# Kernel tuning notes

Hardware: AMD Instinct MI355X
Metric: run time of the kernel (lower is better)

## Reference

```python
import jax, jax.numpy as jnp
import numpy as np

B, T, D, H = 2, 2048, 1024, 16


def setup_inputs() -> dict:
    key = jax.random.key(0)
    kx, kq, kk, kv, ko = jax.random.split(key, 5)
    s = D ** -0.5  # linear-layer init scale
    return {
        "x": jax.random.normal(kx, (B, T, D), dtype=jnp.float32),
        "Wq": jax.random.normal(kq, (D, D), dtype=jnp.float32) * s,
        "Wk": jax.random.normal(kk, (D, D), dtype=jnp.float32) * s,
        "Wv": jax.random.normal(kv, (D, D), dtype=jnp.float32) * s,
        "Wo": jax.random.normal(ko, (D, D), dtype=jnp.float32) * s,
        "quadrant_weights": jnp.array([1.0, -0.5, -0.5, 0.25], dtype=jnp.float32),
    }


def reference(x, Wq, Wk, Wv, Wo, quadrant_weights):
    Bx, Tx, Dx = x.shape
    d = Dx // H          # head dim
    h = d // 2           # quadrant (half-head) dim
    scale = h ** -0.5

    # projections -> (B, H, T, d)
    q = (x @ Wq).reshape(Bx, Tx, H, d).transpose(0, 2, 1, 3)
    k = (x @ Wk).reshape(Bx, Tx, H, d).transpose(0, 2, 1, 3)
    v = (x @ Wv).reshape(Bx, Tx, H, d).transpose(0, 2, 1, 3)

    q1, q2 = q[..., :h], q[..., h:]
    k1, k2 = k[..., :h], k[..., h:]

    w = jax.nn.softmax(quadrant_weights)
    # Fused quadrant sum: w0*q1k1^T + w1*q1k2^T + w2*q2k1^T + w3*q2k2^T
    # == q1 @ (w0*k1 + w1*k2)^T + q2 @ (w2*k1 + w3*k2)^T  (same math, fewer matmuls)
    k_eff1 = w[0] * k1 + w[1] * k2
    k_eff2 = w[2] * k1 + w[3] * k2
    attn = (jnp.einsum('bhqc,bhkc->bhqk', q1, k_eff1)
            + jnp.einsum('bhqc,bhkc->bhqk', q2, k_eff2)) * scale
    attn = jax.nn.softmax(attn, axis=-1)

    out = jnp.einsum('bhqk,bhkd->bhqd', attn, v)
    out = out.transpose(0, 2, 1, 3).reshape(Bx, Tx, Dx)
    return out @ Wo
```

## Files before the change

kernel.cpp:

```cpp
#include <hip/hip_runtime.h>

typedef unsigned short u16;
typedef unsigned int u32;
typedef __attribute__((ext_vector_type(8))) short short8;
typedef __attribute__((ext_vector_type(4))) short short4v;
typedef __attribute__((ext_vector_type(4))) float f32x4;
typedef __attribute__((ext_vector_type(16))) float f32x16;
typedef __attribute__((ext_vector_type(2))) unsigned u32x2;
typedef __attribute__((ext_vector_type(4))) unsigned u32x4;

__device__ __forceinline__ u16 f2bf(float f) {
  union { float f; unsigned u; } a; a.f = f;
  unsigned u = a.u + 0x7fffu + ((a.u >> 16) & 1u);
  return (u16)(u >> 16);
}

__device__ __forceinline__ u32 cvtpk(float lo, float hi_) {
  u32 r; asm("v_cvt_pk_bf16_f32 %0, %1, %2" : "=v"(r) : "v"(lo), "v"(hi_)); return r;
}
__device__ __forceinline__ short8 as_short8(u32x4 v) {
  union { u32x4 u; short8 s; } c; c.u = v; return c.s;
}
__device__ __forceinline__ u32 sh32(u32 v) {
  return (u32)__shfl_xor((int)v, 32, 64);
}
__device__ __forceinline__ float max3f(float a, float b, float c) {
  return fmaxf(fmaxf(a, b), c);
}
__device__ __forceinline__ void gload16(const u16* g, u16* l) {
  __builtin_amdgcn_global_load_lds(
      (__attribute__((address_space(1))) void*)(u16*)g,
      (__attribute__((address_space(3))) void*)l, 16, 0, 0);
}
__device__ __forceinline__ void keep8(short8 v) {
  union { short8 s; int i[4]; } u; u.s = v;
  asm volatile("" :: "v"(u.i[0]), "v"(u.i[1]), "v"(u.i[2]), "v"(u.i[3]));
}
__device__ __forceinline__ void wait_vm4() {
  asm volatile("s_waitcnt vmcnt(4)" ::: "memory");
}
__device__ __forceinline__ void wait_vm3() {
  asm volatile("s_waitcnt vmcnt(3)" ::: "memory");
}
__device__ __forceinline__ void wait_vm0() {
  asm volatile("s_waitcnt vmcnt(0)" ::: "memory");
}
__device__ __forceinline__ void barrier_raw() {
  __builtin_amdgcn_sched_barrier(0);
  __builtin_amdgcn_s_barrier();
  __builtin_amdgcn_sched_barrier(0);
}

__global__ void cvt_x_kernel(const float* __restrict__ x, u16* __restrict__ xb) {
  int i = (blockIdx.x * 256 + threadIdx.x) * 8;
  float4 a = *(const float4*)(x + i);
  float4 b = *(const float4*)(x + i + 4);
  short8 v;
  v[0] = (short)f2bf(a.x); v[1] = (short)f2bf(a.y);
  v[2] = (short)f2bf(a.z); v[3] = (short)f2bf(a.w);
  v[4] = (short)f2bf(b.x); v[5] = (short)f2bf(b.y);
  v[6] = (short)f2bf(b.z); v[7] = (short)f2bf(b.w);
  *(short8*)(xb + i) = v;
}

__global__ void prep_w_kernel(const float* __restrict__ Wq, const float* __restrict__ Wk,
                              const float* __restrict__ Wv, const float* __restrict__ Wo,
                              const float* __restrict__ qw,
                              u16* __restrict__ Wcat, u16* __restrict__ Wot) {
  __shared__ float tile[32][33];
  const int z = blockIdx.z;
  const int n0 = blockIdx.x * 32, k0 = blockIdx.y * 32;
  const float* src = (z == 0) ? Wq : (z == 1) ? Wk : (z == 2) ? Wv : Wo;
  float w0 = 0.f, w1 = 0.f, w2 = 0.f, w3 = 0.f;
  if (z == 1) {
    float a = qw[0], b = qw[1], c = qw[2], d = qw[3];
    float mx = fmaxf(fmaxf(a, b), fmaxf(c, d));
    float ea = expf(a - mx), eb = expf(b - mx), ec = expf(c - mx), ed = expf(d - mx);
    float s = ea + eb + ec + ed;
    w0 = ea / s; w1 = eb / s; w2 = ec / s; w3 = ed / s;
  }
  #pragma unroll
  for (int i = 0; i < 32; i += 8) {
    int k = k0 + threadIdx.y + i;
    int n = n0 + threadIdx.x;
    float v;
    if (z == 1) {
      int c = n & 63;
      if (c < 32) v = w0 * src[k * 1024 + n]      + w1 * src[k * 1024 + n + 32];
      else        v = w2 * src[k * 1024 + n - 32] + w3 * src[k * 1024 + n];
    } else {
      v = src[k * 1024 + n];
    }
    tile[threadIdx.y + i][threadIdx.x] = v;
  }
  __syncthreads();
  #pragma unroll
  for (int i = 0; i < 32; i += 8) {
    int n = n0 + threadIdx.y + i;
    int k = k0 + threadIdx.x;
    u16 v = f2bf(tile[threadIdx.x][threadIdx.y + i]);
    if (z < 3) Wcat[(size_t)(z * 1024 + n) * 1024 + k] = v;
    else       Wot[(size_t)n * 1024 + k] = v;
  }
}

template<int MODE, int BM>
__global__ __launch_bounds__(256, 2)
void gemm_k(const u16* __restrict__ A, const u16* __restrict__ Bm,
            u16* __restrict__ out_q, u16* __restrict__ out_k,
            u16* __restrict__ out_vt, float* __restrict__ out_f) {
  constexpr int WM = BM / 2;
  constexpr int MR = WM / 16;
  __shared__ u16 At[3][BM * 32];
  __shared__ u16 Bt[3][128 * 32];
  const int tid = threadIdx.x;
  const int wid = tid >> 6, lane = tid & 63;
  const int l15 = lane & 15, l4 = lane >> 4;

  const int nwg = gridDim.x * gridDim.y;
  const int cpx = nwg >> 3;
  int bid = blockIdx.y * gridDim.x + blockIdx.x;
  int wg = (bid & 7) * cpx + (bid >> 3);
  const int bx = wg % gridDim.x, by = wg / gridDim.x;
  const int mblk = by * BM, nblk = bx * 128;
  const int wm = (wid >> 1) * WM, wn = (wid & 1) * 64;
  f32x4 acc[MR][4] = {};

  const int rr = lane >> 2;
  const int cA = (lane & 3) * 8;
  const u16* gB = Bm + (size_t)(nblk + wid * 32 + rr) * 1024 + cA;
  const u16* gA = (BM == 128) ? A + (size_t)(mblk + wid * 32 + rr) * 1024 + cA
                              : A + (size_t)(mblk + wid * 16 + rr) * 1024 + cA;

  auto STAGE = [&](int ib, int kt) {
    if constexpr (BM == 128) {
      #pragma unroll
      for (int q = 0; q < 2; ++q)
        gload16(gA + (size_t)q * 16 * 1024 + kt, &At[ib][(wid * 32 + q * 16) * 32]);
    } else {
      gload16(gA + kt, &At[ib][(wid * 16) * 32]);
    }
    #pragma unroll
    for (int q = 0; q < 2; ++q)
      gload16(gB + (size_t)q * 16 * 1024 + kt, &Bt[ib][(wid * 32 + q * 16) * 32]);
  };

  STAGE(0, 0);
  STAGE(1, 32);
  int ib = 0, ibw = 2;
  for (int s = 0; s < 32; ++s) {
    if (s < 31) { if constexpr (BM == 128) wait_vm4(); else wait_vm3(); }
    else wait_vm0();
    barrier_raw();
    if (s + 2 < 32) STAGE(ibw, (s + 2) * 32);
    short8 af[MR], bf[4];
    #pragma unroll
    for (int i = 0; i < MR; ++i)
      af[i] = *(const short8*)(&At[ib][(wm + i * 16 + l15) * 32 + l4 * 8]);
    #pragma unroll
    for (int j = 0; j < 4; ++j)
      bf[j] = *(const short8*)(&Bt[ib][(wn + j * 16 + l15) * 32 + l4 * 8]);
    #pragma unroll
    for (int i = 0; i < MR; ++i)
      #pragma unroll
      for (int j = 0; j < 4; ++j)
        acc[i][j] = __builtin_amdgcn_mfma_f32_16x16x32_bf16(af[i], bf[j], acc[i][j], 0, 0, 0);
    ib = (ib == 2) ? 0 : ib + 1;
    ibw = (ibw == 2) ? 0 : ibw + 1;
  }

  const float QSCALE = 0.17677669529663687f * 1.4426950408889634f;
  #pragma unroll
  for (int i = 0; i < MR; ++i) {
    int m_g = mblk + wm + i * 16 + l4 * 4;
    #pragma unroll
    for (int j = 0; j < 4; ++j) {
      int n_g = nblk + wn + j * 16 + l15;
      f32x4 v = acc[i][j];
      if (MODE == 1) {
        #pragma unroll
        for (int jj = 0; jj < 4; ++jj)
          out_f[(size_t)(m_g + jj) * 1024 + n_g] = v[jj];
      } else {
        if (n_g < 2048) {
          u16* dst; float sc;
          if (n_g < 1024) { dst = out_q; sc = QSCALE; } else { dst = out_k; sc = 1.0f; }
          int nn = n_g & 1023;
          #pragma unroll
          for (int jj = 0; jj < 4; ++jj)
            dst[(size_t)(m_g + jj) * 1024 + nn] = f2bf(v[jj] * sc);
        } else {
          int c = n_g - 2048;
          int b = m_g >> 11, t = m_g & 2047;
          short4v p;
          p[0] = (short)f2bf(v[0]); p[1] = (short)f2bf(v[1]);
          p[2] = (short)f2bf(v[2]); p[3] = (short)f2bf(v[3]);
          *(short4v*)(out_vt + ((size_t)((b << 4) + (c >> 6)) * 64 + (c & 63)) * 2048 + t) = p;
        }
      }
    }
  }
}

__global__ __launch_bounds__(256)
void attn_k(const u16* __restrict__ Q, const u16* __restrict__ Kb,
            const u16* __restrict__ Vt, u16* __restrict__ O) {
  __shared__ u16 lk[3][64 * 64];
  __shared__ u16 lv[3][64 * 64];
  const int tid = threadIdx.x, wid = tid >> 6, lane = tid & 63;
  const int l31 = lane & 31, hi = lane >> 5;

  int bid = blockIdx.y * 16 + blockIdx.x;
  int wg = (bid & 7) * 64 + (bid >> 3);
  const int qt = wg & 15, bh = wg >> 4;
  const int b = bh >> 4, h = bh & 15;
  const int qrow = qt * 128 + wid * 32 + l31;

  short8 qf[4];
  #pragma unroll
  for (int cs = 0; cs < 4; ++cs)
    qf[cs] = *(const short8*)(Q + (size_t)(b * 2048 + qrow) * 1024 + h * 64 + cs * 16 + hi * 8);
  #pragma unroll
  for (int cs = 0; cs < 4; ++cs) keep8(qf[cs]);

  const int sr = lane >> 3;
  const int sc8 = (lane & 7) ^ sr;
  const u16* Kg = Kb + (size_t)b * 2048 * 1024 + h * 64 + sc8 * 8;
  const u16* Vg = Vt + (size_t)bh * 64 * 2048 + sc8 * 8;
  const int s0i = wid * 2;
  const int swz = l31 & 7;

  short8 onesf;
  #pragma unroll
  for (int j = 0; j < 8; ++j) onesf[j] = (short)0x3F80;

  f32x16 accO0 = {}, accO1 = {}, sacc = {};
  float mrun = -1e30f;

  auto STAGE = [&](int tt, int ibx) {
    #pragma unroll
    for (int s2 = 0; s2 < 2; ++s2) {
      int s = s0i + s2;
      int r = s * 8 + sr;
      gload16(Kg + (size_t)(tt * 64 + r) * 1024, &lk[ibx][s * 512]);
      gload16(Vg + (size_t)r * 2048 + tt * 64, &lv[ibx][s * 512]);
    }
  };

  STAGE(0, 0);
  STAGE(1, 1);
  int ib = 0, ibw = 2;

  for (int t = 0; t < 32; ++t) {
    if (t < 31) wait_vm4(); else wait_vm0();
    barrier_raw();
    if (t + 2 < 32) STAGE(t + 2, ibw);

    const u16* kb = lk[ib];
    const u16* vb = lv[ib];

    f32x16 s0v = {}, s1v = {};
    __builtin_amdgcn_s_setprio(1);
    #pragma unroll
    for (int cs = 0; cs < 4; ++cs) {
      int ch = cs * 2 + hi;
      short8 k0 = *(const short8*)(kb + l31 * 64 + ((ch ^ swz) * 8));
      short8 k1 = *(const short8*)(kb + (32 + l31) * 64 + ((ch ^ swz) * 8));
      s0v = __builtin_amdgcn_mfma_f32_32x32x16_bf16(k0, qf[cs], s0v, 0, 0, 0);
      s1v = __builtin_amdgcn_mfma_f32_32x32x16_bf16(k1, qf[cs], s1v, 0, 0, 0);
    }
    __builtin_amdgcn_s_setprio(0);

    float m01 = max3f(s0v[0], s0v[1], s0v[2]);
    float m02 = max3f(s0v[3], s0v[4], s0v[5]);
    float m03 = max3f(s0v[6], s0v[7], s0v[8]);
    float m04 = max3f(s0v[9], s0v[10], s0v[11]);
    float m05 = max3f(s0v[12], s0v[13], s0v[14]);
    float m11 = max3f(s1v[0], s1v[1], s1v[2]);
    float m12 = max3f(s1v[3], s1v[4], s1v[5]);
    float m13 = max3f(s1v[6], s1v[7], s1v[8]);
    float m14 = max3f(s1v[9], s1v[10], s1v[11]);
    float m15 = max3f(s1v[12], s1v[13], s1v[14]);
    float ma = max3f(m01, m02, m03);
    float mb = max3f(m04, m05, s0v[15]);
    float mc = max3f(m11, m12, m13);
    float md = max3f(m14, m15, s1v[15]);
    float mx = fmaxf(fmaxf(ma, mb), fmaxf(mc, md));
    mx = fmaxf(mx, __shfl_xor(mx, 32, 64));

    if (!__all(mx <= mrun + 8.0f)) {
      float mnew = fmaxf(mrun, mx);
      float al = exp2f(mrun - mnew);
      mrun = mnew;
      sacc[0] *= al;
      #pragma unroll
      for (int i = 0; i < 16; ++i) { accO0[i] *= al; accO1[i] *= al; }
    }

    #pragma unroll
    for (int i = 0; i < 16; ++i) { s0v[i] = exp2f(s0v[i] - mrun); s1v[i] = exp2f(s1v[i] - mrun); }

    short8 paS[4];
    #pragma unroll
    for (int half = 0; half < 2; ++half) {
      #pragma unroll
      for (int kq = 0; kq < 2; ++kq) {
        float p0, p1, p2, p3, p4, p5, p6, p7;
        if (half == 0) {
          p0 = s0v[kq*8+0]; p1 = s0v[kq*8+1]; p2 = s0v[kq*8+2]; p3 = s0v[kq*8+3];
          p4 = s0v[kq*8+4]; p5 = s0v[kq*8+5]; p6 = s0v[kq*8+6]; p7 = s0v[kq*8+7];
        } else {
          p0 = s1v[kq*8+0]; p1 = s1v[kq*8+1]; p2 = s1v[kq*8+2]; p3 = s1v[kq*8+3];
          p4 = s1v[kq*8+4]; p5 = s1v[kq*8+5]; p6 = s1v[kq*8+6]; p7 = s1v[kq*8+7];
        }
        u32 A = cvtpk(p0, p1), B = cvtpk(p2, p3);
        u32 C = cvtpk(p4, p5), D = cvtpk(p6, p7);
        u32 e1 = sh32(hi ? A : C);
        u32 e2 = sh32(hi ? B : D);
        u32x4 w;
        w[0] = hi ? e1 : A;
        w[1] = hi ? e2 : B;
        w[2] = hi ? C : e1;
        w[3] = hi ? D : e2;
        paS[half * 2 + kq] = as_short8(w);
      }
    }

    __builtin_amdgcn_s_setprio(1);
    #pragma unroll
    for (int ks = 0; ks < 4; ++ks) {
      int ch = ks * 2 + hi;
      short8 v0 = *(const short8*)(vb + l31 * 64 + ((ch ^ swz) * 8));
      short8 v1 = *(const short8*)(vb + (32 + l31) * 64 + ((ch ^ swz) * 8));
      accO0 = __builtin_amdgcn_mfma_f32_32x32x16_bf16(v0, paS[ks], accO0, 0, 0, 0);
      accO1 = __builtin_amdgcn_mfma_f32_32x32x16_bf16(v1, paS[ks], accO1, 0, 0, 0);
      sacc  = __builtin_amdgcn_mfma_f32_32x32x16_bf16(onesf, paS[ks], sacc, 0, 0, 0);
    }
    __builtin_amdgcn_s_setprio(0);

    ib = (ib == 2) ? 0 : ib + 1;
    ibw = (ibw == 2) ? 0 : ibw + 1;
  }

  float inv = 1.0f / sacc[0];
  u16* Op = O + (size_t)(b * 2048 + qrow) * 1024 + h * 64;
  #pragma unroll
  for (int g = 0; g < 4; ++g) {
    u32x2 pr;
    pr[0] = cvtpk(accO0[4*g] * inv, accO0[4*g+1] * inv);
    pr[1] = cvtpk(accO0[4*g+2] * inv, accO0[4*g+3] * inv);
    *(u32x2*)(Op + 8*g + 4*hi) = pr;
    u32x2 pr2;
    pr2[0] = cvtpk(accO1[4*g] * inv, accO1[4*g+1] * inv);
    pr2[1] = cvtpk(accO1[4*g+2] * inv, accO1[4*g+3] * inv);
    *(u32x2*)(Op + 32 + 8*g + 4*hi) = pr2;
  }
}

extern "C" void kernel_launch(void* const* d_in, const int* in_sizes, int n_in,
                              void* d_out, int out_size, void* d_ws, size_t ws_size,
                              hipStream_t stream) {
  const float* x  = (const float*)d_in[0];
  const float* Wq = (const float*)d_in[1];
  const float* Wk = (const float*)d_in[2];
  const float* Wv = (const float*)d_in[3];
  const float* Wo = (const float*)d_in[4];
  const float* qw = (const float*)d_in[5];

  char* w = (char*)d_ws;
  u16* xb   = (u16*)(w);
  u16* Wcat = (u16*)(w + (8u  << 20));
  u16* Wot  = (u16*)(w + (14u << 20));
  u16* Qb   = (u16*)(w + (16u << 20));
  u16* Kb   = (u16*)(w + (24u << 20));
  u16* Vtb  = (u16*)(w + (32u << 20));
  u16* Ob   = (u16*)(w + (40u << 20));

  cvt_x_kernel<<<2048, 256, 0, stream>>>(x, xb);
  prep_w_kernel<<<dim3(32, 32, 4), dim3(32, 8), 0, stream>>>(Wq, Wk, Wv, Wo, qw, Wcat, Wot);
  gemm_k<0, 128><<<dim3(24, 32), 256, 0, stream>>>(xb, Wcat, Qb, Kb, Vtb, nullptr);
  attn_k<<<dim3(16, 32), 256, 0, stream>>>(Qb, Kb, Vtb, Ob);
  gemm_k<1, 64><<<dim3(8, 64), 256, 0, stream>>>(Ob, Wot, nullptr, nullptr, nullptr, (float*)d_out);
}
```

Measured before the change: 138.7 us.

## Split attention over two KV halves and merge partials in a separate kernel

```diff
diff --git a/kernel.cpp b/kernel.cpp
--- a/kernel.cpp
+++ b/kernel.cpp
@@ -14,7 +14,10 @@
   unsigned u = a.u + 0x7fffu + ((a.u >> 16) & 1u);
   return (u16)(u >> 16);
 }
-
+__device__ __forceinline__ float bf2f(short s) {
+  union { unsigned u; float f; } a; a.u = ((unsigned)(unsigned short)s) << 16;
+  return a.f;
+}
 __device__ __forceinline__ u32 cvtpk(float lo, float hi_) {
   u32 r; asm("v_cvt_pk_bf16_f32 %0, %1, %2" : "=v"(r) : "v"(lo), "v"(hi_)); return r;
 }
@@ -36,15 +39,9 @@
   union { short8 s; int i[4]; } u; u.s = v;
   asm volatile("" :: "v"(u.i[0]), "v"(u.i[1]), "v"(u.i[2]), "v"(u.i[3]));
 }
-__device__ __forceinline__ void wait_vm4() {
-  asm volatile("s_waitcnt vmcnt(4)" ::: "memory");
-}
-__device__ __forceinline__ void wait_vm3() {
-  asm volatile("s_waitcnt vmcnt(3)" ::: "memory");
-}
-__device__ __forceinline__ void wait_vm0() {
-  asm volatile("s_waitcnt vmcnt(0)" ::: "memory");
-}
+__device__ __forceinline__ void wait_vm4() { asm volatile("s_waitcnt vmcnt(4)" ::: "memory"); }
+__device__ __forceinline__ void wait_vm3() { asm volatile("s_waitcnt vmcnt(3)" ::: "memory"); }
+__device__ __forceinline__ void wait_vm0() { asm volatile("s_waitcnt vmcnt(0)" ::: "memory"); }
 __device__ __forceinline__ void barrier_raw() {
   __builtin_amdgcn_sched_barrier(0);
   __builtin_amdgcn_s_barrier();
@@ -202,17 +199,20 @@
   }
 }
 
-__global__ __launch_bounds__(256)
+__global__ __launch_bounds__(256, 4)
 void attn_k(const u16* __restrict__ Q, const u16* __restrict__ Kb,
-            const u16* __restrict__ Vt, u16* __restrict__ O) {
-  __shared__ u16 lk[3][64 * 64];
-  __shared__ u16 lv[3][64 * 64];
+            const u16* __restrict__ Vt, u16* __restrict__ Opart,
+            float* __restrict__ ML) {
+  __shared__ u16 lk[2][64 * 64];
+  __shared__ u16 lv[2][64 * 64];
   const int tid = threadIdx.x, wid = tid >> 6, lane = tid & 63;
   const int l31 = lane & 31, hi = lane >> 5;
 
   int bid = blockIdx.y * 16 + blockIdx.x;
-  int wg = (bid & 7) * 64 + (bid >> 3);
-  const int qt = wg & 15, bh = wg >> 4;
+  int wg = (bid & 7) * 128 + (bid >> 3);
+  const int qt = wg & 15;
+  const int yy = wg >> 4;
+  const int half = yy & 1, bh = yy >> 1;
   const int b = bh >> 4, h = bh & 15;
   const int qrow = qt * 128 + wid * 32 + l31;
 
@@ -225,8 +225,8 @@
 
   const int sr = lane >> 3;
   const int sc8 = (lane & 7) ^ sr;
-  const u16* Kg = Kb + (size_t)b * 2048 * 1024 + h * 64 + sc8 * 8;
-  const u16* Vg = Vt + (size_t)bh * 64 * 2048 + sc8 * 8;
+  const u16* Kg = Kb + ((size_t)b * 2048 + half * 1024) * 1024 + h * 64 + sc8 * 8;
+  const u16* Vg = Vt + (size_t)bh * 64 * 2048 + half * 1024 + sc8 * 8;
   const int s0i = wid * 2;
   const int swz = l31 & 7;
 
@@ -248,16 +248,14 @@
   };
 
   STAGE(0, 0);
-  STAGE(1, 1);
-  int ib = 0, ibw = 2;
-
-  for (int t = 0; t < 32; ++t) {
-    if (t < 31) wait_vm4(); else wait_vm0();
+
+  for (int t = 0; t < 16; ++t) {
+    wait_vm0();
     barrier_raw();
-    if (t + 2 < 32) STAGE(t + 2, ibw);
-
-    const u16* kb = lk[ib];
-    const u16* vb = lv[ib];
+    if (t + 1 < 16) STAGE(t + 1, (t + 1) & 1);
+
+    const u16* kb = lk[t & 1];
+    const u16* vb = lv[t & 1];
 
     f32x16 s0v = {}, s1v = {};
     __builtin_amdgcn_s_setprio(1);
@@ -302,11 +300,11 @@
 
     short8 paS[4];
     #pragma unroll
-    for (int half = 0; half < 2; ++half) {
+    for (int hf = 0; hf < 2; ++hf) {
       #pragma unroll
       for (int kq = 0; kq < 2; ++kq) {
         float p0, p1, p2, p3, p4, p5, p6, p7;
-        if (half == 0) {
+        if (hf == 0) {
           p0 = s0v[kq*8+0]; p1 = s0v[kq*8+1]; p2 = s0v[kq*8+2]; p3 = s0v[kq*8+3];
           p4 = s0v[kq*8+4]; p5 = s0v[kq*8+5]; p6 = s0v[kq*8+6]; p7 = s0v[kq*8+7];
         } else {
@@ -322,7 +320,7 @@
         w[1] = hi ? e2 : B;
         w[2] = hi ? C : e1;
         w[3] = hi ? D : e2;
-        paS[half * 2 + kq] = as_short8(w);
+        paS[hf * 2 + kq] = as_short8(w);
       }
     }
 
@@ -337,24 +335,54 @@
       sacc  = __builtin_amdgcn_mfma_f32_32x32x16_bf16(onesf, paS[ks], sacc, 0, 0, 0);
     }
     __builtin_amdgcn_s_setprio(0);
-
-    ib = (ib == 2) ? 0 : ib + 1;
-    ibw = (ibw == 2) ? 0 : ibw + 1;
-  }
-
-  float inv = 1.0f / sacc[0];
-  u16* Op = O + (size_t)(b * 2048 + qrow) * 1024 + h * 64;
+  }
+
+  u16* Po = Opart + (size_t)(half * 4096 + b * 2048 + qrow) * 1024 + h * 64;
   #pragma unroll
   for (int g = 0; g < 4; ++g) {
     u32x2 pr;
-    pr[0] = cvtpk(accO0[4*g] * inv, accO0[4*g+1] * inv);
-    pr[1] = cvtpk(accO0[4*g+2] * inv, accO0[4*g+3] * inv);
-    *(u32x2*)(Op + 8*g + 4*hi) = pr;
+    pr[0] = cvtpk(accO0[4*g],     accO0[4*g+1]);
+    pr[1] = cvtpk(accO0[4*g+2],   accO0[4*g+3]);
+    *(u32x2*)(Po + 8*g + 4*hi) = pr;
     u32x2 pr2;
-    pr2[0] = cvtpk(accO1[4*g] * inv, accO1[4*g+1] * inv);
-    pr2[1] = cvtpk(accO1[4*g+2] * inv, accO1[4*g+3] * inv);
-    *(u32x2*)(Op + 32 + 8*g + 4*hi) = pr2;
-  }
+    pr2[0] = cvtpk(accO1[4*g],    accO1[4*g+1]);
+    pr2[1] = cvtpk(accO1[4*g+2],  accO1[4*g+3]);
+    *(u32x2*)(Po + 32 + 8*g + 4*hi) = pr2;
+  }
+  if (hi == 0) {
+    float2 v; v.x = mrun; v.y = sacc[0];
+    ((float2*)ML)[(size_t)(half * 32 + bh) * 2048 + qrow] = v;
+  }
+}
+
+__global__ __launch_bounds__(256)
+void merge_k(const u16* __restrict__ Opart, const float* __restrict__ ML,
+             u16* __restrict__ Ob) {
+  int i = blockIdx.x * 256 + threadIdx.x;
+  int e = i * 8;
+  int row = e >> 10;
+  int col = e & 1023;
+  int h = col >> 6;
+  int b = row >> 11;
+  int tr = row & 2047;
+  int bh = b * 16 + h;
+  const float2* ml = (const float2*)ML;
+  float2 x1 = ml[(size_t)bh * 2048 + tr];
+  float2 x2 = ml[(size_t)(32 + bh) * 2048 + tr];
+  float M = fmaxf(x1.x, x2.x);
+  float a1 = exp2f(x1.x - M), a2 = exp2f(x2.x - M);
+  float inv = 1.0f / (x1.y * a1 + x2.y * a2);
+  float f1 = a1 * inv, f2 = a2 * inv;
+  short8 o1 = *(const short8*)(Opart + (size_t)row * 1024 + col);
+  short8 o2 = *(const short8*)(Opart + (size_t)(4096 + row) * 1024 + col);
+  u32x4 w;
+  #pragma unroll
+  for (int j = 0; j < 4; ++j) {
+    float lo = bf2f(o1[2*j])   * f1 + bf2f(o2[2*j])   * f2;
+    float hi_ = bf2f(o1[2*j+1]) * f1 + bf2f(o2[2*j+1]) * f2;
+    w[j] = cvtpk(lo, hi_);
+  }
+  *(u32x4*)(Ob + (size_t)row * 1024 + col) = w;
 }
 
 extern "C" void kernel_launch(void* const* d_in, const int* in_sizes, int n_in,
@@ -368,17 +396,20 @@
   const float* qw = (const float*)d_in[5];
 
   char* w = (char*)d_ws;
-  u16* xb   = (u16*)(w);
-  u16* Wcat = (u16*)(w + (8u  << 20));
-  u16* Wot  = (u16*)(w + (14u << 20));
-  u16* Qb   = (u16*)(w + (16u << 20));
-  u16* Kb   = (u16*)(w + (24u << 20));
-  u16* Vtb  = (u16*)(w + (32u << 20));
-  u16* Ob   = (u16*)(w + (40u << 20));
+  u16* Wot   = (u16*)(w);
+  u16* Qb    = (u16*)(w + (2u  << 20));
+  u16* Kb    = (u16*)(w + (10u << 20));
+  u16* Vtb   = (u16*)(w + (18u << 20));
+  u16* xb    = (u16*)(w + (26u << 20));
+  u16* Wcat  = (u16*)(w + (34u << 20));
+  u16* Opart = (u16*)(w + (26u << 20));
+  float* ML  = (float*)(w + (42u << 20));
+  u16* Ob    = Qb;
 
   cvt_x_kernel<<<2048, 256, 0, stream>>>(x, xb);
   prep_w_kernel<<<dim3(32, 32, 4), dim3(32, 8), 0, stream>>>(Wq, Wk, Wv, Wo, qw, Wcat, Wot);
   gemm_k<0, 128><<<dim3(24, 32), 256, 0, stream>>>(xb, Wcat, Qb, Kb, Vtb, nullptr);
-  attn_k<<<dim3(16, 32), 256, 0, stream>>>(Qb, Kb, Vtb, Ob);
+  attn_k<<<dim3(16, 64), 256, 0, stream>>>(Qb, Kb, Vtb, Opart, ML);
+  merge_k<<<2048, 256, 0, stream>>>(Opart, ML, Ob);
   gemm_k<1, 64><<<dim3(8, 64), 256, 0, stream>>>(Ob, Wot, nullptr, nullptr, nullptr, (float*)d_out);
 }
```

Result: slower. 142.3 us (+2.6%).

## Switch GEMM to double-buffered BK=64 tiles with XOR-swizzled LDS layout

Applied to the files above, without the earlier changes.

```diff
diff --git a/kernel.cpp b/kernel.cpp
--- a/kernel.cpp
+++ b/kernel.cpp
@@ -14,7 +14,6 @@
   unsigned u = a.u + 0x7fffu + ((a.u >> 16) & 1u);
   return (u16)(u >> 16);
 }
-
 __device__ __forceinline__ u32 cvtpk(float lo, float hi_) {
   u32 r; asm("v_cvt_pk_bf16_f32 %0, %1, %2" : "=v"(r) : "v"(lo), "v"(hi_)); return r;
 }
@@ -36,15 +35,8 @@
   union { short8 s; int i[4]; } u; u.s = v;
   asm volatile("" :: "v"(u.i[0]), "v"(u.i[1]), "v"(u.i[2]), "v"(u.i[3]));
 }
-__device__ __forceinline__ void wait_vm4() {
-  asm volatile("s_waitcnt vmcnt(4)" ::: "memory");
-}
-__device__ __forceinline__ void wait_vm3() {
-  asm volatile("s_waitcnt vmcnt(3)" ::: "memory");
-}
-__device__ __forceinline__ void wait_vm0() {
-  asm volatile("s_waitcnt vmcnt(0)" ::: "memory");
-}
+__device__ __forceinline__ void wait_vm4() { asm volatile("s_waitcnt vmcnt(4)" ::: "memory"); }
+__device__ __forceinline__ void wait_vm0() { asm volatile("s_waitcnt vmcnt(0)" ::: "memory"); }
 __device__ __forceinline__ void barrier_raw() {
   __builtin_amdgcn_sched_barrier(0);
   __builtin_amdgcn_s_barrier();
@@ -111,8 +103,9 @@
             u16* __restrict__ out_vt, float* __restrict__ out_f) {
   constexpr int WM = BM / 2;
   constexpr int MR = WM / 16;
-  __shared__ u16 At[3][BM * 32];
-  __shared__ u16 Bt[3][128 * 32];
+  constexpr int AQ = BM / 32;
+  __shared__ u16 At[2][BM * 64];
+  __shared__ u16 Bt[2][128 * 64];
   const int tid = threadIdx.x;
   const int wid = tid >> 6, lane = tid & 63;
   const int l15 = lane & 15, l4 = lane >> 4;
@@ -126,47 +119,48 @@
   const int wm = (wid >> 1) * WM, wn = (wid & 1) * 64;
   f32x4 acc[MR][4] = {};
 
-  const int rr = lane >> 2;
-  const int cA = (lane & 3) * 8;
-  const u16* gB = Bm + (size_t)(nblk + wid * 32 + rr) * 1024 + cA;
-  const u16* gA = (BM == 128) ? A + (size_t)(mblk + wid * 32 + rr) * 1024 + cA
-                              : A + (size_t)(mblk + wid * 16 + rr) * 1024 + cA;
+  const int r8 = lane >> 3;
+  const int sc8 = (lane & 7) ^ r8;
+  const u16* gA = A  + (size_t)(mblk + wid * (BM / 4) + r8) * 1024 + sc8 * 8;
+  const u16* gB = Bm + (size_t)(nblk + wid * 32 + r8) * 1024 + sc8 * 8;
 
   auto STAGE = [&](int ib, int kt) {
-    if constexpr (BM == 128) {
-      #pragma unroll
-      for (int q = 0; q < 2; ++q)
-        gload16(gA + (size_t)q * 16 * 1024 + kt, &At[ib][(wid * 32 + q * 16) * 32]);
-    } else {
-      gload16(gA + kt, &At[ib][(wid * 16) * 32]);
-    }
-    #pragma unroll
-    for (int q = 0; q < 2; ++q)
-      gload16(gB + (size_t)q * 16 * 1024 + kt, &Bt[ib][(wid * 32 + q * 16) * 32]);
+    #pragma unroll
+    for (int q = 0; q < AQ; ++q)
+      gload16(gA + (size_t)q * 8 * 1024 + kt, &At[ib][(wid * (BM / 4) + q * 8) * 64]);
+    #pragma unroll
+    for (int q = 0; q < 4; ++q)
+      gload16(gB + (size_t)q * 8 * 1024 + kt, &Bt[ib][(wid * 32 + q * 8) * 64]);
   };
 
   STAGE(0, 0);
-  STAGE(1, 32);
-  int ib = 0, ibw = 2;
-  for (int s = 0; s < 32; ++s) {
-    if (s < 31) { if constexpr (BM == 128) wait_vm4(); else wait_vm3(); }
-    else wait_vm0();
+  wait_vm0();
+  barrier_raw();
+  int ib = 0;
+  for (int t = 0; t < 16; ++t) {
+    if (t < 15) STAGE(ib ^ 1, (t + 1) * 64);
+    short8 af[MR][2], bf[4][2];
+    #pragma unroll
+    for (int kk = 0; kk < 2; ++kk) {
+      #pragma unroll
+      for (int i = 0; i < MR; ++i)
+        af[i][kk] = *(const short8*)(&At[ib][(wm + i * 16 + l15) * 64
+                                             + (((kk * 4 + l4) ^ (l15 & 7)) * 8)]);
+      #pragma unroll
+      for (int j = 0; j < 4; ++j)
+        bf[j][kk] = *(const short8*)(&Bt[ib][(wn + j * 16 + l15) * 64
+                                             + (((kk * 4 + l4) ^ (l15 & 7)) * 8)]);
+    }
+    #pragma unroll
+    for (int kk = 0; kk < 2; ++kk)
+      #pragma unroll
+      for (int i = 0; i < MR; ++i)
+        #pragma unroll
+        for (int j = 0; j < 4; ++j)
+          acc[i][j] = __builtin_amdgcn_mfma_f32_16x16x32_bf16(af[i][kk], bf[j][kk], acc[i][j], 0, 0, 0);
+    wait_vm0();
     barrier_raw();
-    if (s + 2 < 32) STAGE(ibw, (s + 2) * 32);
-    short8 af[MR], bf[4];
-    #pragma unroll
-    for (int i = 0; i < MR; ++i)
-      af[i] = *(const short8*)(&At[ib][(wm + i * 16 + l15) * 32 + l4 * 8]);
-    #pragma unroll
-    for (int j = 0; j < 4; ++j)
-      bf[j] = *(const short8*)(&Bt[ib][(wn + j * 16 + l15) * 32 + l4 * 8]);
-    #pragma unroll
-    for (int i = 0; i < MR; ++i)
-      #pragma unroll
-      for (int j = 0; j < 4; ++j)
-        acc[i][j] = __builtin_amdgcn_mfma_f32_16x16x32_bf16(af[i], bf[j], acc[i][j], 0, 0, 0);
-    ib = (ib == 2) ? 0 : ib + 1;
-    ibw = (ibw == 2) ? 0 : ibw + 1;
+    ib ^= 1;
   }
 
   const float QSCALE = 0.17677669529663687f * 1.4426950408889634f;
```

After: 153.5 us. 1.11x slower.
